# Optimization experiments

Measured on AMD Instinct MI355X. Metric: run time of the kernel, lower is better.

The kernel has to match this reference:

```python
import jax, jax.numpy as jnp
import numpy as np

EPS = 1e-12  # torch F.normalize eps

def _l2norm(x):
    n = jnp.linalg.norm(x, axis=1, keepdims=True)
    return x / jnp.maximum(n, EPS)

def setup_inputs() -> dict:
    key = jax.random.key(0)
    kq, km = jax.random.split(key)
    queries = jax.random.normal(kq, (4096, 128), dtype=jnp.float32)
    memory = jax.random.normal(km, (100000, 128), dtype=jnp.float32)
    return {"queries": queries, "memory": memory, "k": 3}

def reference(queries, memory, k):
    q = _l2norm(queries)                      # [N, D]
    m = _l2norm(memory)                       # [M, D]
    sims = q @ m.T                            # [N, M]
    values, indices = jax.lax.top_k(sims, k)  # [N, k] each
    distances = 1.0 - values
    return distances, indices
```

## Files before the change

kernel.cpp:

```cpp
#include <hip/hip_runtime.h>
#include <hip/hip_bf16.h>

typedef unsigned short u16;
typedef unsigned int u32;

#define N_Q 4096
#define N_M 100000
#define N_M_PAD 100096
#define DDIM 128
#define QTILE 128
#define MTILE 64
#define NCHUNK 24
#define NQT (N_Q / QTILE)
#define TOTAL_MT (N_M_PAD / MTILE)
#define TPC ((TOTAL_MT + NCHUNK - 1) / NCHUNK)
#define NCAND (NCHUNK * 2 * 3)

typedef short bf16x8 __attribute__((ext_vector_type(8)));
typedef float f32x4 __attribute__((ext_vector_type(4)));

static __device__ __forceinline__ u16 f2bf(float v) {
  union { float f; u32 u; } a; a.f = v;
  u32 r = a.u + 0x7fffu + ((a.u >> 16) & 1u);
  return (u16)(r >> 16);
}

static __device__ __forceinline__ void async_copy16(const u16* gp, u16* lp) {
  __builtin_amdgcn_global_load_lds(
      (const __attribute__((address_space(1))) u32*)gp,
      (__attribute__((address_space(3))) u32*)lp, 16, 0, 0);
}

__global__ __launch_bounds__(256) void knorm(const float* __restrict__ q, const float* __restrict__ m,
                                             u16* __restrict__ qn, u16* __restrict__ mn,
                                             float* __restrict__ qinv, float* __restrict__ minv) {
  const int lane = threadIdx.x & 63;
  const int nw = gridDim.x * 4;
  for (int row = blockIdx.x * 4 + (threadIdx.x >> 6); row < N_Q + N_M_PAD; row += nw) {
    const float* src;
    u16* dst;
    int mr = 0;
    bool is_q = (row < N_Q);
    bool pad = false;
    if (is_q) {
      src = q + (size_t)row * DDIM;
      dst = qn + (size_t)row * DDIM;
    } else {
      mr = row - N_Q;
      pad = (mr >= N_M);
      src = m + (size_t)mr * DDIM;
      dst = mn + (size_t)mr * DDIM;
    }
    float2 x;
    if (pad) { x.x = 0.f; x.y = 0.f; }
    else x = ((const float2*)src)[lane];
    float s = x.x * x.x + x.y * x.y;
    #pragma unroll
    for (int off = 1; off < 64; off <<= 1) s += __shfl_xor(s, off, 64);
    float invn = 1.0f / fmaxf(sqrtf(s), 1e-12f);
    u32 packed = (u32)f2bf(x.x * invn) | ((u32)f2bf(x.y * invn) << 16);
    ((u32*)dst)[lane] = packed;
    if (lane == 0) {
      if (is_q) qinv[row] = invn;
      else minv[mr] = pad ? 0.f : invn;
    }
  }
}

static __device__ __forceinline__ void stage4(const u16* __restrict__ mn, u16* dst,
                                              int t, const u32* goff, u32 loff0) {
  const u16* gbase = mn + (size_t)t * MTILE * DDIM;
  #pragma unroll
  for (int it = 0; it < 4; ++it)
    async_copy16(gbase + goff[it], dst + loff0 + (u32)(it * 64) * 8);
}

static __device__ __forceinline__ void tileWork(
    const u16* As, int tl, int wm, int quad, int l15,
    const bf16x8 (&bq)[4][4], float (&tv0)[4], float (&tv1)[4], float (&tv2)[4]) {
  f32x4 acc[2][4];
  {
    int c = quad ^ l15;
    bf16x8 a0 = *(const bf16x8*)&As[((wm * 32 + l15) * 16 + c) * 8];
    bf16x8 a1 = *(const bf16x8*)&As[((wm * 32 + 16 + l15) * 16 + c) * 8];
    f32x4 z = {0.f, 0.f, 0.f, 0.f};
    #pragma unroll
    for (int ni = 0; ni < 4; ++ni) {
      acc[0][ni] = __builtin_amdgcn_mfma_f32_16x16x32_bf16(a0, bq[ni][0], z, 0, 0, 0);
      acc[1][ni] = __builtin_amdgcn_mfma_f32_16x16x32_bf16(a1, bq[ni][0], z, 0, 0, 0);
    }
  }
  #pragma unroll
  for (int s = 1; s < 4; ++s) {
    int c = (s * 4 + quad) ^ l15;
    bf16x8 a0 = *(const bf16x8*)&As[((wm * 32 + l15) * 16 + c) * 8];
    bf16x8 a1 = *(const bf16x8*)&As[((wm * 32 + 16 + l15) * 16 + c) * 8];
    #pragma unroll
    for (int ni = 0; ni < 4; ++ni) {
      acc[0][ni] = __builtin_amdgcn_mfma_f32_16x16x32_bf16(a0, bq[ni][s], acc[0][ni], 0, 0, 0);
      acc[1][ni] = __builtin_amdgcn_mfma_f32_16x16x32_bf16(a1, bq[ni][s], acc[1][ni], 0, 0, 0);
    }
  }
  const u32 cb = ((u32)tl << 3) | ((u32)quad << 1);
  #pragma unroll
  for (int ni = 0; ni < 4; ++ni) {
    #pragma unroll
    for (int mi = 0; mi < 2; ++mi) {
      f32x4 x = acc[mi][ni];
      float M = fmaxf(fmaxf(x[0], x[1]), fmaxf(x[2], x[3]));
      float pk = __uint_as_float((__float_as_uint(M) & 0xFFFFFC00u) | (cb | (u32)mi));
      tv2[ni] = __builtin_amdgcn_fmed3f(tv1[ni], tv2[ni], pk);
      tv1[ni] = __builtin_amdgcn_fmed3f(tv0[ni], tv1[ni], pk);
      tv0[ni] = fmaxf(tv0[ni], pk);
    }
  }
}

__global__ __launch_bounds__(256, 3) void kgemm(const u16* __restrict__ qn,
                                                const u16* __restrict__ mn,
                                                float* __restrict__ pval) {
  __shared__ u16 B0[MTILE * DDIM];
  __shared__ u16 B1[MTILE * DDIM];
  __shared__ u16 B2[MTILE * DDIM];

  const int id = blockIdx.x;
  const int xcd = id & 7, sub = id >> 3;
  const int ch = xcd * 3 + (sub >> 5);
  const int qt = sub & 31;
  const int tid = threadIdx.x;
  const int wid = tid >> 6, lane = tid & 63;
  const int quad = lane >> 4, l15 = lane & 15;
  const int wm = wid >> 1, wq = wid & 1;

  const int t0 = ch * TPC;
  const int t1 = (t0 + TPC < TOTAL_MT) ? (t0 + TPC) : TOTAL_MT;
  const int nt = t1 - t0;

  u32 goff[4];
  u32 loff0;
  {
    int u0 = wid * 256 + lane;
    loff0 = (u32)(wid * 256) * 8;
    #pragma unroll
    for (int it = 0; it < 4; ++it) {
      int u = u0 + it * 64;
      int row = u >> 4, su = u & 15;
      int k8 = su ^ (row & 15);
      goff[it] = (u32)(row * DDIM + k8 * 8);
    }
  }

  bf16x8 bq[4][4];
  #pragma unroll
  for (int ni = 0; ni < 4; ++ni) {
    int col = qt * QTILE + wq * 64 + ni * 16 + l15;
    #pragma unroll
    for (int s = 0; s < 4; ++s)
      bq[ni][s] = *(const bf16x8*)&qn[(size_t)col * DDIM + (s * 4 + quad) * 8];
  }

  stage4(mn, B0, t0 + 0, goff, loff0);
  stage4(mn, B1, t0 + 1, goff, loff0);

  float tv0[4], tv1[4], tv2[4];
  #pragma unroll
  for (int i = 0; i < 4; ++i) { tv0[i] = tv1[i] = tv2[i] = -1e30f; }

  asm volatile("s_waitcnt vmcnt(4)" ::: "memory");
  asm volatile("s_barrier" ::: "memory");

  int r = 0;
  #define ROUND(BC, BS)                                                        \
    {                                                                          \
      int ts = t0 + r + 2;                                                     \
      ts = (ts < t1) ? ts : (t1 - 1);                                          \
      stage4(mn, BS, ts, goff, loff0);                                         \
      tileWork(BC, r, wm, quad, l15, bq, tv0, tv1, tv2);                       \
      asm volatile("s_waitcnt vmcnt(4)" ::: "memory");                         \
      asm volatile("s_barrier" ::: "memory");                                  \
      ++r;                                                                     \
      if (r >= nt) break;                                                      \
    }
  while (true) {
    ROUND(B0, B2)
    ROUND(B1, B0)
    ROUND(B2, B1)
  }
  #undef ROUND

  #pragma unroll
  for (int ni = 0; ni < 4; ++ni) {
    float a0 = tv0[ni], a1 = tv1[ni], a2 = tv2[ni];
    #pragma unroll
    for (int off = 16; off <= 32; off <<= 1) {
      float b0 = __shfl_xor(a0, off, 64);
      float b1 = __shfl_xor(a1, off, 64);
      float b2 = __shfl_xor(a2, off, 64);
      float n0 = fmaxf(a0, b0);
      float n1 = __builtin_amdgcn_fmed3f(a0, b0, fmaxf(a1, b1));
      float n2 = fmaxf(fmaxf(fminf(a1, b0), fminf(a0, b1)), fmaxf(a2, b2));
      a0 = n0; a1 = n1; a2 = n2;
    }
    float v = (quad == 0) ? a0 : ((quad == 1) ? a1 : a2);
    if (quad < 3) {
      int qlocal = wq * 64 + ni * 16 + l15;
      size_t base = (((size_t)qt * NCHUNK + ch) * QTILE + qlocal) * 6 + wm * 3 + quad;
      pval[base] = v;
    }
  }
}

__global__ __launch_bounds__(256) void kmerge(const float* __restrict__ pval,
                                              const float* __restrict__ q,
                                              const float* __restrict__ mem,
                                              const float* __restrict__ qinv,
                                              const float* __restrict__ minv,
                                              float* __restrict__ out) {
  __shared__ float sv[4][32];
  const int tid = threadIdx.x;
  const int wqd = tid >> 6;
  const int lane = tid & 63;
  const int qg = blockIdx.x * 4 + wqd;
  const int qt = qg >> 7, ql = qg & 127;

  const int c0 = lane * 3;
  float cv[3] = {-1e31f, -1e31f, -1e31f};
  if (c0 < NCAND) {
    int chn = c0 / 6, rem = c0 - chn * 6;
    size_t b = (((size_t)qt * NCHUNK + chn) * QTILE + ql) * 6 + rem;
    cv[0] = pval[b];
    cv[1] = pval[b + 1];
    cv[2] = pval[b + 2];
  }

  float wv[8]; int wp[8];
  #pragma unroll
  for (int pass = 0; pass < 8; ++pass) {
    float bv = cv[0]; int bp = c0;
    #pragma unroll
    for (int j = 1; j < 3; ++j) {
      bool g = (cv[j] > bv);
      bv = g ? cv[j] : bv; bp = g ? (c0 + j) : bp;
    }
    #pragma unroll
    for (int off = 32; off >= 1; off >>= 1) {
      float ov = __shfl_xor(bv, off, 64);
      int op = __shfl_xor(bp, off, 64);
      bool g = (ov > bv) || (ov == bv && op < bp);
      bv = g ? ov : bv; bp = g ? op : bp;
    }
    wv[pass] = bv; wp[pass] = bp;
    #pragma unroll
    for (int j = 0; j < 3; ++j)
      if (c0 + j == bp) cv[j] = -1e31f;
  }

  const float qi = qinv[qg];
  const float* qrow = q + (size_t)qg * DDIM;

  const int p = lane >> 3, e = (lane >> 1) & 3, h = lane & 1;
  float bvv = wv[0]; int bpp = wp[0];
  #pragma unroll
  for (int k = 1; k < 8; ++k) {
    bvv = (p == k) ? wv[k] : bvv;
    bpp = (p == k) ? wp[k] : bpp;
  }
  {
    u32 code = __float_as_uint(bvv) & 1023u;
    int chn = bpp / 6;
    int wm = (bpp - chn * 6) / 3;
    int tl = (int)(code >> 3), qd = (int)((code >> 1) & 3u), mi = (int)(code & 1u);
    int row = (chn * TPC + tl) * MTILE + wm * 32 + mi * 16 + qd * 4 + e;
    bool valid = (row < N_M);
    int ra = valid ? row : 0;
    const float* mrow = mem + (size_t)ra * DDIM;
    float s = 0.f;
    #pragma unroll
    for (int i = 0; i < 16; ++i) {
      float4 mv = *(const float4*)&mrow[h * 64 + i * 4];
      float4 qv = *(const float4*)&qrow[h * 64 + i * 4];
      s += qv.x * mv.x + qv.y * mv.y + qv.z * mv.z + qv.w * mv.w;
    }
    s += __shfl_xor(s, 1, 64);
    s = valid ? (s * qi * minv[ra]) : -1e30f;
    if (h == 0) sv[wqd][p * 4 + e] = s;
  }
  __syncthreads();

  float myv = (lane < 32) ? sv[wqd][lane] : -1e31f;
  int myrow;
  {
    int p2 = lane >> 2, e2 = lane & 3;
    float bv2 = wv[0]; int bp2 = wp[0];
    #pragma unroll
    for (int k = 1; k < 8; ++k) {
      bool sel = (p2 == k);
      bv2 = sel ? wv[k] : bv2;
      bp2 = sel ? wp[k] : bp2;
    }
    u32 code = __float_as_uint(bv2) & 1023u;
    int chn = bp2 / 6;
    int wm = (bp2 - chn * 6) / 3;
    int tl = (int)(code >> 3), qd = (int)((code >> 1) & 3u), mi = (int)(code & 1u);
    int row = (chn * TPC + tl) * MTILE + wm * 32 + mi * 16 + qd * 4 + e2;
    myrow = (lane < 32 && row < N_M) ? row : (N_M + lane);
    if (lane >= 32 || row >= N_M) myv = -1e31f;
  }

  #pragma unroll
  for (int a = 0; a < 3; ++a) {
    float bv = myv; int bi = myrow;
    #pragma unroll
    for (int off = 32; off >= 1; off >>= 1) {
      float ov = __shfl_xor(bv, off, 64);
      int oi = __shfl_xor(bi, off, 64);
      bool g2 = (ov > bv) || (ov == bv && oi < bi);
      bv = g2 ? ov : bv; bi = g2 ? oi : bi;
    }
    if (lane == 0) {
      out[(size_t)qg * 3 + a] = 1.0f - bv;
      out[(size_t)N_Q * 3 + (size_t)qg * 3 + a] = (float)bi;
    }
    if (myrow == bi) myv = -1e31f;
  }
}

extern "C" void kernel_launch(void* const* d_in, const int* in_sizes, int n_in,
                              void* d_out, int out_size, void* d_ws, size_t ws_size,
                              hipStream_t stream) {
  const float* q = (const float*)d_in[0];
  const float* m = (const float*)d_in[1];

  char* ws = (char*)d_ws;
  size_t off = 0;
  u16* qn = (u16*)(ws + off); off += (size_t)N_Q * DDIM * 2;
  u16* mn = (u16*)(ws + off); off += (size_t)N_M_PAD * DDIM * 2;
  float* qinv = (float*)(ws + off); off += (size_t)N_Q * 4;
  float* minv = (float*)(ws + off); off += (size_t)N_M_PAD * 4;
  float* pval = (float*)(ws + off); off += (size_t)N_Q * NCAND * 4;

  knorm<<<2048, 256, 0, stream>>>(q, m, qn, mn, qinv, minv);
  kgemm<<<NQT * NCHUNK, 256, 0, stream>>>(qn, mn, pval);
  kmerge<<<N_Q / 4, 256, 0, stream>>>(pval, q, m, qinv, minv, (float*)d_out);
}
```

Baseline: 219.3 us.

## Software-pipeline MFMA tile with previous tile's top-k epilogue

Splits the per-tile work into an MFMA phase and a top-3 epilogue phase, then double-buffers the accumulators so each round issues the current tile's MFMAs and runs the previous tile's epilogue. This lets the VALU max/med3 work overlap the matrix-core latency instead of waiting on the accumulators right after the MFMAs. The cost is doubled accumulator registers (32 extra VGPRs), which could hurt occupancy under the launch bound of 3. The loop is unrolled to six rounds to handle the rotation of both the buffers and the accumulators.

```diff
diff --git a/kernel.cpp b/kernel.cpp
--- a/kernel.cpp
+++ b/kernel.cpp
@@ -75,10 +75,9 @@
     async_copy16(gbase + goff[it], dst + loff0 + (u32)(it * 64) * 8);
 }
 
-static __device__ __forceinline__ void tileWork(
-    const u16* As, int tl, int wm, int quad, int l15,
-    const bf16x8 (&bq)[4][4], float (&tv0)[4], float (&tv1)[4], float (&tv2)[4]) {
-  f32x4 acc[2][4];
+static __device__ __forceinline__ void mfmaTile(
+    const u16* As, int wm, int quad, int l15,
+    const bf16x8 (&bq)[4][4], f32x4 (&acc)[2][4]) {
   {
     int c = quad ^ l15;
     bf16x8 a0 = *(const bf16x8*)&As[((wm * 32 + l15) * 16 + c) * 8];
@@ -101,6 +100,11 @@
       acc[1][ni] = __builtin_amdgcn_mfma_f32_16x16x32_bf16(a1, bq[ni][s], acc[1][ni], 0, 0, 0);
     }
   }
+}
+
+static __device__ __forceinline__ void epiTile(
+    const f32x4 (&acc)[2][4], int tl, int quad,
+    float (&tv0)[4], float (&tv1)[4], float (&tv2)[4]) {
   const u32 cb = ((u32)tl << 3) | ((u32)quad << 1);
   #pragma unroll
   for (int ni = 0; ni < 4; ++ni) {
@@ -166,27 +170,41 @@
   #pragma unroll
   for (int i = 0; i < 4; ++i) { tv0[i] = tv1[i] = tv2[i] = -1e30f; }
 
+  f32x4 accA[2][4], accB[2][4];
+
   asm volatile("s_waitcnt vmcnt(4)" ::: "memory");
   asm volatile("s_barrier" ::: "memory");
 
-  int r = 0;
-  #define ROUND(BC, BS)                                                        \
+  stage4(mn, B2, t0 + 2, goff, loff0);
+  mfmaTile(B0, wm, quad, l15, bq, accA);
+  asm volatile("s_waitcnt vmcnt(4)" ::: "memory");
+  asm volatile("s_barrier" ::: "memory");
+
+  int r = 1;
+  #define ROUND(BC, BS, CUR, PRV)                                              \
     {                                                                          \
       int ts = t0 + r + 2;                                                     \
       ts = (ts < t1) ? ts : (t1 - 1);                                          \
       stage4(mn, BS, ts, goff, loff0);                                         \
-      tileWork(BC, r, wm, quad, l15, bq, tv0, tv1, tv2);                       \
+      mfmaTile(BC, wm, quad, l15, bq, CUR);                                    \
+      epiTile(PRV, r - 1, quad, tv0, tv1, tv2);                                \
       asm volatile("s_waitcnt vmcnt(4)" ::: "memory");                         \
       asm volatile("s_barrier" ::: "memory");                                  \
       ++r;                                                                     \
       if (r >= nt) break;                                                      \
     }
   while (true) {
-    ROUND(B0, B2)
-    ROUND(B1, B0)
-    ROUND(B2, B1)
+    ROUND(B1, B0, accB, accA)
+    ROUND(B2, B1, accA, accB)
+    ROUND(B0, B2, accB, accA)
+    ROUND(B1, B0, accA, accB)
+    ROUND(B2, B1, accB, accA)
+    ROUND(B0, B2, accA, accB)
   }
   #undef ROUND
+
+  if ((nt - 1) & 1) epiTile(accB, nt - 1, quad, tv0, tv1, tv2);
+  else              epiTile(accA, nt - 1, quad, tv0, tv1, tv2);
 
   #pragma unroll
   for (int ni = 0; ni < 4; ++ni) {
```

Result: slower. 251.8 us (+14.8%).
